# Kernel tuning notes

Measured on AMD Instinct MI355X. Metric: run time of the kernel, lower is better.

## Reference

```python
import jax, jax.numpy as jnp
import numpy as np

NL, D, NH, HD, MLP, L = 4, 1280, 16, 80, 5120, 2048
SEG = 512  # patches per packed image


def setup_inputs() -> dict:
    key = jax.random.key(0)
    ks = jax.random.split(key, 16)
    s = 0.02
    # per-segment RoPE frequency table: positions restart at each image boundary
    inv_freq = 1.0 / (10000.0 ** (jnp.arange(0, HD, 2, dtype=jnp.float32) / HD))  # (HD/2,)
    pos = (jnp.arange(L) % SEG).astype(jnp.float32)
    rotary_pos_emb = pos[:, None] * inv_freq[None, :]  # (L, HD/2)
    return {
        "x": jax.random.normal(ks[0], (L, D), jnp.float32),
        "rotary_pos_emb": rotary_pos_emb,
        "cu_seqlens": jnp.array([0, 512, 1024, 1536, 2048], jnp.int32),
        "ln1_g": 1.0 + s * jax.random.normal(ks[1], (NL, D), jnp.float32),
        "ln1_b": s * jax.random.normal(ks[2], (NL, D), jnp.float32),
        "ln2_g": 1.0 + s * jax.random.normal(ks[3], (NL, D), jnp.float32),
        "ln2_b": s * jax.random.normal(ks[4], (NL, D), jnp.float32),
        "qkv_w": s * jax.random.normal(ks[5], (NL, 3 * D, D), jnp.float32),
        "qkv_b": s * jax.random.normal(ks[6], (NL, 3 * D), jnp.float32),
        "proj_w": s * jax.random.normal(ks[7], (NL, D, D), jnp.float32),
        "proj_b": s * jax.random.normal(ks[8], (NL, D), jnp.float32),
        "mlp_w1": s * jax.random.normal(ks[9], (NL, MLP, D), jnp.float32),
        "mlp_b1": s * jax.random.normal(ks[10], (NL, MLP), jnp.float32),
        "mlp_w2": s * jax.random.normal(ks[11], (NL, D, MLP), jnp.float32),
        "mlp_b2": s * jax.random.normal(ks[12], (NL, D), jnp.float32),
    }


def _ln(x, g, b):
    m = jnp.mean(x, axis=-1, keepdims=True)
    v = jnp.mean((x - m) ** 2, axis=-1, keepdims=True)
    return (x - m) * jax.lax.rsqrt(v + 1e-6) * g + b


def _rope(t, cos, sin):
    # t: (L, H, HD); cos/sin: (L, 1, HD)
    half = t.shape[-1] // 2
    rot = jnp.concatenate([-t[..., half:], t[..., :half]], axis=-1)
    return t * cos + rot * sin


def reference(x, rotary_pos_emb, cu_seqlens, ln1_g, ln1_b, ln2_g, ln2_b,
              qkv_w, qkv_b, proj_w, proj_b, mlp_w1, mlp_b1, mlp_w2, mlp_b2):
    Lx = x.shape[0]
    cos = jnp.cos(rotary_pos_emb)
    sin = jnp.sin(rotary_pos_emb)
    cos = jnp.concatenate([cos, cos], axis=-1)[:, None, :]  # (L,1,HD)
    sin = jnp.concatenate([sin, sin], axis=-1)[:, None, :]
    # block-diagonal attention mask from cu_seqlens via segment ids
    seg = jnp.searchsorted(cu_seqlens, jnp.arange(Lx), side="right")  # (L,)
    mask = seg[:, None] == seg[None, :]  # (L,L) bool
    neg = jnp.finfo(jnp.float32).min
    scale = 1.0 / np.sqrt(HD)
    for l in range(qkv_w.shape[0]):
        h = _ln(x, ln1_g[l], ln1_b[l])
        qkv = (h @ qkv_w[l].T + qkv_b[l]).reshape(Lx, 3, NH, HD)
        q, k, v = qkv[:, 0], qkv[:, 1], qkv[:, 2]  # (L,H,HD) each
        q = _rope(q, cos, sin)
        k = _rope(k, cos, sin)
        scores = jnp.einsum("lhd,mhd->hlm", q, k) * scale  # (H,L,L)
        scores = jnp.where(mask[None], scores, neg)
        w = jax.nn.softmax(scores.astype(jnp.float32), axis=-1).astype(x.dtype)
        att = jnp.einsum("hlm,mhd->lhd", w, v).reshape(Lx, NH * HD)
        x = x + att @ proj_w[l].T + proj_b[l]
        h = _ln(x, ln2_g[l], ln2_b[l])
        x = x + jax.nn.gelu(h @ mlp_w1[l].T + mlp_b1[l], approximate=True) @ mlp_w2[l].T + mlp_b2[l]
    return x
```

## Files before the change

### kernel.cpp

```cpp
#include <hip/hip_runtime.h>
#include <cstdint>
#include <cstddef>

typedef unsigned short u16;
typedef __bf16 bf16_t;
typedef bf16_t bf16x8 __attribute__((ext_vector_type(8)));
typedef float f32x4 __attribute__((ext_vector_type(4)));

#define NLAY 4
#define DMODEL 1280
#define NHEAD 16
#define HDIM 80
#define HDP 96
#define MLPD 5120
#define LTOK 2048
#define SEGLEN 512

__device__ __forceinline__ u16 f2bf(float f) {
  union { float f; unsigned u; } x; x.f = f;
  unsigned r = x.u + 0x7fffu + ((x.u >> 16) & 1u);
  return (u16)(r >> 16);
}
__device__ __forceinline__ float bf2f(u16 s) {
  union { unsigned u; float f; } x; x.u = ((unsigned)s) << 16;
  return x.f;
}

#define GLOAD_LDS16(gsrc, ldst) \
  __builtin_amdgcn_global_load_lds((const __attribute__((address_space(1))) void*)(gsrc), \
                                   (__attribute__((address_space(3))) void*)(ldst), 16, 0, 0)

__device__ __forceinline__ void barrier_mem() {
  asm volatile("s_barrier" ::: "memory");
}

#define C0 (3 * DMODEL * DMODEL / 4)
#define C1 (C0 + DMODEL * DMODEL / 4)
#define C2 (C1 + MLPD * DMODEL / 4)
#define C3 (C2 + DMODEL * MLPD / 4)
__global__ __launch_bounds__(256) void cvt4(const float* __restrict__ s_q,
                                            const float* __restrict__ s_p,
                                            const float* __restrict__ s_1,
                                            const float* __restrict__ s_2,
                                            u16* __restrict__ o_q, u16* __restrict__ o_p,
                                            u16* __restrict__ o_1, u16* __restrict__ o_2) {
  int i = blockIdx.x * 256 + threadIdx.x;
  const float* src; u16* dst; int off;
  if (i < C0)      { src = s_q; dst = o_q; off = i; }
  else if (i < C1) { src = s_p; dst = o_p; off = i - C0; }
  else if (i < C2) { src = s_1; dst = o_1; off = i - C1; }
  else if (i < C3) { src = s_2; dst = o_2; off = i - C2; }
  else return;
  const float4 v = reinterpret_cast<const float4*>(src)[off];
  union { u16 s[4]; uint2 u; } o;
  o.s[0] = f2bf(v.x); o.s[1] = f2bf(v.y); o.s[2] = f2bf(v.z); o.s[3] = f2bf(v.w);
  reinterpret_cast<uint2*>(dst)[off] = o.u;
}

__global__ __launch_bounds__(256) void ln_bf16(const float* __restrict__ x,
                                               const float* __restrict__ g,
                                               const float* __restrict__ b,
                                               u16* __restrict__ out) {
  int row = blockIdx.x;
  int t = threadIdx.x;
  const float* xr = x + (size_t)row * DMODEL;
  float v[5]; float s = 0.f, s2 = 0.f;
#pragma unroll
  for (int i = 0; i < 5; i++) { v[i] = xr[t + i * 256]; s += v[i]; s2 += v[i] * v[i]; }
#pragma unroll
  for (int off = 32; off; off >>= 1) { s += __shfl_down(s, off); s2 += __shfl_down(s2, off); }
  __shared__ float ps[4], ps2[4];
  int w = t >> 6;
  if ((t & 63) == 0) { ps[w] = s; ps2[w] = s2; }
  __syncthreads();
  s = ps[0] + ps[1] + ps[2] + ps[3];
  s2 = ps2[0] + ps2[1] + ps2[2] + ps2[3];
  float mean = s * (1.f / DMODEL);
  float var = s2 * (1.f / DMODEL) - mean * mean;
  float inv = rsqrtf(var + 1e-6f);
#pragma unroll
  for (int i = 0; i < 5; i++) {
    int c = t + i * 256;
    out[(size_t)row * DMODEL + c] = f2bf((v[i] - mean) * inv * g[c] + b[c]);
  }
}

__global__ __launch_bounds__(256) void reduce_ln(const u16* __restrict__ P,
                                                 const float* __restrict__ bias,
                                                 float* __restrict__ x,
                                                 const float* __restrict__ g,
                                                 const float* __restrict__ b,
                                                 u16* __restrict__ out) {
  int row = blockIdx.x;
  int t = threadIdx.x;
  const size_t PS = (size_t)LTOK * DMODEL;
  const size_t base = (size_t)row * DMODEL;
  float v[5]; float s = 0.f, s2 = 0.f;
#pragma unroll
  for (int i = 0; i < 5; i++) {
    int c = t + i * 256;
    float val = x[base + c] + bias[c];
#pragma unroll
    for (int z = 0; z < 4; z++) val += bf2f(P[z * PS + base + c]);
    x[base + c] = val;
    v[i] = val; s += val; s2 += val * val;
  }
#pragma unroll
  for (int off = 32; off; off >>= 1) { s += __shfl_down(s, off); s2 += __shfl_down(s2, off); }
  __shared__ float ps[4], ps2[4];
  int w = t >> 6;
  if ((t & 63) == 0) { ps[w] = s; ps2[w] = s2; }
  __syncthreads();
  s = ps[0] + ps[1] + ps[2] + ps[3];
  s2 = ps2[0] + ps2[1] + ps2[2] + ps2[3];
  float mean = s * (1.f / DMODEL);
  float var = s2 * (1.f / DMODEL) - mean * mean;
  float inv = rsqrtf(var + 1e-6f);
#pragma unroll
  for (int i = 0; i < 5; i++) {
    int c = t + i * 256;
    out[base + c] = f2bf((v[i] - mean) * inv * g[c] + b[c]);
  }
}

template <int EPI>
__global__ __launch_bounds__(512, 4) void gemmhp(const u16* __restrict__ A,
                                                 const u16* __restrict__ B,
                                                 const float* __restrict__ bias,
                                                 u16* __restrict__ Cb,
                                                 int M, int N, int K) {
  __shared__ u16 As[3][128 * 32];
  __shared__ u16 Bs[3][256 * 32];

  int gN = gridDim.x, gM = gridDim.y;
  int flat = blockIdx.x + gN * blockIdx.y;
  int nwg = gN * gM;
  int qc = nwg >> 3, rc = nwg & 7;
  int xcd = flat & 7, pos = flat >> 3;
  int start = (xcd < rc) ? xcd * (qc + 1) : rc * (qc + 1) + (xcd - rc) * qc;
  int swz = start + pos;
  int m0 = (swz % gM) * 128;
  int n0 = (swz / gM) * 256;

  int t = threadIdx.x, lane = t & 63, w = t >> 6;
  int wm = w >> 2, wn = w & 3;
  int r = lane & 15, kq = lane >> 4;
  f32x4 acc[4][4] = {};

  auto stageA = [&](int buf, int k0) {
    int row = t >> 2, s = t & 3;
    int ss = s ^ ((row >> 1) & 3);
    GLOAD_LDS16(A + (size_t)(m0 + row) * K + k0 + ss * 8, &As[buf][t * 8]);
  };
  auto stageB = [&](int buf, int k0) {
#pragma unroll
    for (int i = 0; i < 2; i++) {
      int chunk = i * 512 + t;
      int row = chunk >> 2, s = chunk & 3;
      int ss = s ^ ((row >> 1) & 3);
      GLOAD_LDS16(B + (size_t)(n0 + row) * K + k0 + ss * 8, &Bs[buf][chunk * 8]);
    }
  };

  int NT = K >> 5;
  stageA(0, 0); stageB(0, 0);
  stageA(1, 32); stageB(1, 32);

  int bt = 0;
  for (int kt = 0; kt < NT; kt++) {
    if (kt == NT - 1) asm volatile("s_waitcnt vmcnt(0)" ::: "memory");
    else              asm volatile("s_waitcnt vmcnt(3)" ::: "memory");
    barrier_mem();
    const u16* as = As[bt];
    const u16* bs = Bs[bt];
    int b2 = bt + 2; if (b2 >= 3) b2 -= 3;
    bool st = (kt + 2) < NT;
    int k2 = (kt + 2) << 5;

    bf16x8 af[4], bfv[4];
#pragma unroll
    for (int i = 0; i < 4; i++) {
      int row = wm * 64 + i * 16 + r;
      int ss = kq ^ ((row >> 1) & 3);
      af[i] = *(const bf16x8*)&as[row * 32 + ss * 8];
    }
#pragma unroll
    for (int j = 0; j < 4; j++) {
      int row = wn * 64 + j * 16 + r;
      int ss = kq ^ ((row >> 1) & 3);
      bfv[j] = *(const bf16x8*)&bs[row * 32 + ss * 8];
    }
    if (st) { stageA(b2, k2); stageB(b2, k2); }
    __builtin_amdgcn_s_setprio(1);
#pragma unroll
    for (int i = 0; i < 4; i++)
#pragma unroll
      for (int j = 0; j < 4; j++)
        acc[i][j] = __builtin_amdgcn_mfma_f32_16x16x32_bf16(af[i], bfv[j], acc[i][j], 0, 0, 0);
    __builtin_amdgcn_s_setprio(0);

    bt++; if (bt == 3) bt = 0;
  }

#pragma unroll
  for (int i = 0; i < 4; i++) {
#pragma unroll
    for (int j = 0; j < 4; j++) {
      int col = n0 + wn * 64 + j * 16 + r;
      float bv = bias[col];
#pragma unroll
      for (int reg = 0; reg < 4; reg++) {
        int rowg = m0 + wm * 64 + i * 16 + kq * 4 + reg;
        float val = acc[i][j][reg] + bv;
        if (EPI == 2) {
          float z2 = -1.5957691216057308f * fmaf(0.044715f * val, val * val, val);
          float gg = val / (1.f + __expf(z2));
          Cb[(size_t)rowg * N + col] = f2bf(gg);
        } else {
          Cb[(size_t)rowg * N + col] = f2bf(val);
        }
      }
    }
  }
}

__global__ __launch_bounds__(256, 3) void gemmskb(const u16* __restrict__ A,
                                                  const u16* __restrict__ B,
                                                  u16* __restrict__ P,
                                                  int M, int N, int K, int KC) {
  __shared__ u16 As[3][128 * 32];
  __shared__ u16 Bs[3][128 * 32];

  int gN = gridDim.x, gM = gridDim.y;
  int flat = blockIdx.x + gN * blockIdx.y;
  int nwg = gN * gM;
  int qc = nwg >> 3, rc = nwg & 7;
  int xcd = flat & 7, pos = flat >> 3;
  int start = (xcd < rc) ? xcd * (qc + 1) : rc * (qc + 1) + (xcd - rc) * qc;
  int swz = start + pos;
  int n0 = (swz % gN) * 128;
  int m0 = (swz / gN) * 128;
  int kbase = blockIdx.z * KC;
  u16* Pz = P + (size_t)blockIdx.z * M * N;

  int t = threadIdx.x, lane = t & 63, w = t >> 6;
  int wm = w >> 1, wn = w & 1;
  int r = lane & 15, kq = lane >> 4;
  f32x4 acc[4][4] = {};

  auto stage = [&](int buf, int k0) {
#pragma unroll
    for (int i = 0; i < 2; i++) {
      int chunk = i * 256 + t;
      int row = chunk >> 2, s = chunk & 3;
      int ss = s ^ ((row >> 1) & 3);
      GLOAD_LDS16(A + (size_t)(m0 + row) * K + k0 + ss * 8, &As[buf][chunk * 8]);
    }
#pragma unroll
    for (int i = 0; i < 2; i++) {
      int chunk = i * 256 + t;
      int row = chunk >> 2, s = chunk & 3;
      int ss = s ^ ((row >> 1) & 3);
      GLOAD_LDS16(B + (size_t)(n0 + row) * K + k0 + ss * 8, &Bs[buf][chunk * 8]);
    }
  };

  int NT = KC >> 5;
  stage(0, kbase);
  stage(1, kbase + 32);

  int bt = 0;
  for (int kt = 0; kt < NT; kt++) {
    if (kt == NT - 1) asm volatile("s_waitcnt vmcnt(0)" ::: "memory");
    else              asm volatile("s_waitcnt vmcnt(4)" ::: "memory");
    barrier_mem();
    const u16* as = As[bt];
    const u16* bs = Bs[bt];
    int b2 = bt + 2; if (b2 >= 3) b2 -= 3;
    bool st = (kt + 2) < NT;
    int k2 = kbase + ((kt + 2) << 5);

    bf16x8 af[4], bfv[4];
#pragma unroll
    for (int i = 0; i < 4; i++) {
      int row = wm * 64 + i * 16 + r;
      int ss = kq ^ ((row >> 1) & 3);
      af[i] = *(const bf16x8*)&as[row * 32 + ss * 8];
    }
#pragma unroll
    for (int j = 0; j < 4; j++) {
      int row = wn * 64 + j * 16 + r;
      int ss = kq ^ ((row >> 1) & 3);
      bfv[j] = *(const bf16x8*)&bs[row * 32 + ss * 8];
    }
    if (st) stage(b2, k2);
    __builtin_amdgcn_s_setprio(1);
#pragma unroll
    for (int i = 0; i < 4; i++)
#pragma unroll
      for (int j = 0; j < 4; j++)
        acc[i][j] = __builtin_amdgcn_mfma_f32_16x16x32_bf16(af[i], bfv[j], acc[i][j], 0, 0, 0);
    __builtin_amdgcn_s_setprio(0);

    bt++; if (bt == 3) bt = 0;
  }

#pragma unroll
  for (int i = 0; i < 4; i++) {
#pragma unroll
    for (int j = 0; j < 4; j++) {
      int col = n0 + wn * 64 + j * 16 + r;
#pragma unroll
      for (int reg = 0; reg < 4; reg++) {
        int rowg = m0 + wm * 64 + i * 16 + kq * 4 + reg;
        Pz[(size_t)rowg * N + col] = f2bf(acc[i][j][reg]);
      }
    }
  }
}

#define N8TOT (LTOK * DMODEL / 8)
__global__ __launch_bounds__(256) void reduce4b(const u16* __restrict__ P,
                                                const float* __restrict__ bias,
                                                float4* __restrict__ x) {
  int i = blockIdx.x * 256 + threadIdx.x;
  if (i >= N8TOT) return;
  const size_t PS = (size_t)LTOK * DMODEL;
  float s[8] = {};
#pragma unroll
  for (int z = 0; z < 4; z++) {
    uint4 pv = *reinterpret_cast<const uint4*>(P + z * PS + (size_t)i * 8);
    const u16* ps = (const u16*)&pv;
#pragma unroll
    for (int e = 0; e < 8; e++) s[e] += bf2f(ps[e]);
  }
  int cb = (i % (DMODEL / 8)) * 8;
  float4 b0 = *reinterpret_cast<const float4*>(bias + cb);
  float4 b1 = *reinterpret_cast<const float4*>(bias + cb + 4);
  float4 xv0 = x[i * 2], xv1 = x[i * 2 + 1];
  xv0.x += s[0] + b0.x; xv0.y += s[1] + b0.y;
  xv0.z += s[2] + b0.z; xv0.w += s[3] + b0.w;
  xv1.x += s[4] + b1.x; xv1.y += s[5] + b1.y;
  xv1.z += s[6] + b1.z; xv1.w += s[7] + b1.w;
  x[i * 2] = xv0; x[i * 2 + 1] = xv1;
}

__global__ __launch_bounds__(256) void rope_pack(const u16* __restrict__ qkv,
                                                 const float* __restrict__ rpe,
                                                 u16* __restrict__ qp,
                                                 u16* __restrict__ kp) {
  int l = blockIdx.x;
  int t = threadIdx.x;
  __shared__ float cs[40], sn[40];
  if (t < 40) {
    float a = rpe[l * 40 + t];
    cs[t] = cosf(a);
    sn[t] = sinf(a);
  }
  __syncthreads();
  const u16* row = qkv + (size_t)l * (3 * DMODEL);
  const float scale = 0.11180339887498949f;
#pragma unroll
  for (int i = 0; i < 5; i++) {
    int e = t + i * 256;
    int h = e / HDIM, d = e - h * HDIM;
    int dm = (d < 40) ? d : d - 40;
    float c = cs[dm], s = sn[dm];
    float qv = bf2f(row[h * HDIM + d]);
    float qr = (d < 40) ? -bf2f(row[h * HDIM + d + 40]) : bf2f(row[h * HDIM + d - 40]);
    qp[((size_t)h * LTOK + l) * HDP + d] = f2bf((qv * c + qr * s) * scale);
    float kv = bf2f(row[DMODEL + h * HDIM + d]);
    float kr = (d < 40) ? -bf2f(row[DMODEL + h * HDIM + d + 40]) : bf2f(row[DMODEL + h * HDIM + d - 40]);
    kp[((size_t)h * LTOK + l) * HDP + d] = f2bf(kv * c + kr * s);
  }
  {
    int h = t >> 4, p = t & 15;
    qp[((size_t)h * LTOK + l) * HDP + HDIM + p] = 0;
    kp[((size_t)h * LTOK + l) * HDP + HDIM + p] = 0;
  }
}

__global__ __launch_bounds__(256) void vtrans(const u16* __restrict__ qkv,
                                              u16* __restrict__ vt) {
  int blk = blockIdx.x;
  int h = blk >> 5, lt = blk & 31;
  int t = threadIdx.x;
  __shared__ u16 ld[64][81];
#pragma unroll
  for (int i = 0; i < 20; i++) {
    int idx = t + i * 256;
    int ll = idx / HDIM, d = idx - ll * HDIM;
    ld[ll][d] = qkv[(size_t)(lt * 64 + ll) * (3 * DMODEL) + 2 * DMODEL + h * HDIM + d];
  }
  __syncthreads();
#pragma unroll
  for (int i = 0; i < 20; i++) {
    int idx = t + i * 256;
    int d = idx >> 6, ll = idx & 63;
    vt[((size_t)h * HDIM + d) * LTOK + lt * 64 + ll] = ld[ll][d];
  }
}

__global__ __launch_bounds__(256) void attn(const u16* __restrict__ qp,
                                            const u16* __restrict__ kp,
                                            const u16* __restrict__ vt,
                                            u16* __restrict__ out) {
  int bid = blockIdx.x;
  int h = bid >> 5;
  int seg = (bid >> 3) & 3;
  int qt = bid & 7;
  int t = threadIdx.x, w = t >> 6, lane = t & 63;
  int r = lane & 15, kq = lane >> 4;
  __shared__ u16 P[4][16][512];
  int seg0 = seg * SEGLEN;
  int q0 = seg0 + qt * 64 + w * 16;

  bf16x8 qf[3];
  const u16* qrow = qp + ((size_t)h * LTOK + q0 + r) * HDP;
#pragma unroll
  for (int kk = 0; kk < 3; kk++) qf[kk] = *(const bf16x8*)(qrow + kk * 32 + kq * 8);

  f32x4 sc[32];
#pragma unroll
  for (int j = 0; j < 32; j++) {
    f32x4 a = {0.f, 0.f, 0.f, 0.f};
    const u16* krow = kp + ((size_t)h * LTOK + seg0 + j * 16 + r) * HDP;
#pragma unroll
    for (int kk = 0; kk < 3; kk++) {
      bf16x8 bfr = *(const bf16x8*)(krow + kk * 32 + kq * 8);
      a = __builtin_amdgcn_mfma_f32_16x16x32_bf16(qf[kk], bfr, a, 0, 0, 0);
    }
    sc[j] = a;
  }

#pragma unroll
  for (int rr = 0; rr < 4; rr++) {
    float m = -1e30f;
#pragma unroll
    for (int j = 0; j < 32; j++) m = fmaxf(m, sc[j][rr]);
#pragma unroll
    for (int off = 1; off < 16; off <<= 1) m = fmaxf(m, __shfl_xor(m, off));
    float s = 0.f;
#pragma unroll
    for (int j = 0; j < 32; j++) { float e = __expf(sc[j][rr] - m); sc[j][rr] = e; s += e; }
#pragma unroll
    for (int off = 1; off < 16; off <<= 1) s += __shfl_xor(s, off);
    float inv = 1.f / s;
#pragma unroll
    for (int j = 0; j < 32; j++)
      P[w][kq * 4 + rr][j * 16 + r] = f2bf(sc[j][rr] * inv);
  }
  __syncthreads();

  f32x4 oc[5] = {};
#pragma unroll
  for (int tt = 0; tt < 16; tt++) {
    bf16x8 a = *(const bf16x8*)&P[w][r][tt * 32 + kq * 8];
#pragma unroll
    for (int n = 0; n < 5; n++) {
      const u16* vrow = vt + ((size_t)h * HDIM + n * 16 + r) * LTOK + seg0 + tt * 32 + kq * 8;
      bf16x8 bfr = *(const bf16x8*)vrow;
      oc[n] = __builtin_amdgcn_mfma_f32_16x16x32_bf16(a, bfr, oc[n], 0, 0, 0);
    }
  }
#pragma unroll
  for (int n = 0; n < 5; n++)
#pragma unroll
    for (int reg = 0; reg < 4; reg++) {
      int l = q0 + kq * 4 + reg;
      out[(size_t)l * DMODEL + h * HDIM + n * 16 + r] = f2bf(oc[n][reg]);
    }
}

extern "C" void kernel_launch(void* const* d_in, const int* in_sizes, int n_in,
                              void* d_out, int out_size, void* d_ws, size_t ws_size,
                              hipStream_t stream) {
  (void)in_sizes; (void)n_in; (void)out_size; (void)ws_size;
  const float* x_in   = (const float*)d_in[0];
  const float* rpe    = (const float*)d_in[1];
  const float* ln1_g  = (const float*)d_in[3];
  const float* ln1_b  = (const float*)d_in[4];
  const float* ln2_g  = (const float*)d_in[5];
  const float* ln2_b  = (const float*)d_in[6];
  const float* qkv_w  = (const float*)d_in[7];
  const float* qkv_b  = (const float*)d_in[8];
  const float* proj_w = (const float*)d_in[9];
  const float* proj_b = (const float*)d_in[10];
  const float* mlp_w1 = (const float*)d_in[11];
  const float* mlp_b1 = (const float*)d_in[12];
  const float* mlp_w2 = (const float*)d_in[13];
  const float* mlp_b2 = (const float*)d_in[14];
  float* x = (float*)d_out;

  char* ws = (char*)d_ws;
  size_t off = 0;
  auto alloc = [&](size_t bytes) -> char* {
    char* p = ws + off;
    off = (off + bytes + 255) & ~(size_t)255;
    return p;
  };
  u16* wq  = (u16*)alloc((size_t)3 * DMODEL * DMODEL * 2);
  u16* wp  = (u16*)alloc((size_t)DMODEL * DMODEL * 2);
  u16* w1  = (u16*)alloc((size_t)MLPD * DMODEL * 2);
  u16* w2  = (u16*)alloc((size_t)DMODEL * MLPD * 2);
  u16* hb  = (u16*)alloc((size_t)LTOK * DMODEL * 2);
  u16* qkvb = (u16*)alloc((size_t)LTOK * 3 * DMODEL * 2);
  u16* qp  = (u16*)alloc((size_t)NHEAD * LTOK * HDP * 2);
  u16* kp  = (u16*)alloc((size_t)NHEAD * LTOK * HDP * 2);
  u16* vt  = (u16*)alloc((size_t)NHEAD * HDIM * LTOK * 2);
  u16* att = (u16*)alloc((size_t)LTOK * DMODEL * 2);
  u16* ge  = (u16*)alloc((size_t)LTOK * MLPD * 2);
  u16* pk_proj = ge;
  u16* pk_mlp2 = hb;

  hipMemcpyAsync(x, x_in, (size_t)LTOK * DMODEL * sizeof(float),
                 hipMemcpyDeviceToDevice, stream);

  for (int l = 0; l < NLAY; l++) {
    cvt4<<<(C3 + 255) / 256, 256, 0, stream>>>(
        qkv_w + (size_t)l * 3 * DMODEL * DMODEL, proj_w + (size_t)l * DMODEL * DMODEL,
        mlp_w1 + (size_t)l * MLPD * DMODEL, mlp_w2 + (size_t)l * DMODEL * MLPD,
        wq, wp, w1, w2);

    if (l == 0)
      ln_bf16<<<LTOK, 256, 0, stream>>>(x, ln1_g, ln1_b, hb);
    gemmhp<3><<<dim3(15, 16), 512, 0, stream>>>(
        hb, wq, qkv_b + (size_t)l * 3 * DMODEL, qkvb, LTOK, 3 * DMODEL, DMODEL);
    rope_pack<<<LTOK, 256, 0, stream>>>(qkvb, rpe, qp, kp);
    vtrans<<<NHEAD * 32, 256, 0, stream>>>(qkvb, vt);
    attn<<<NHEAD * 4 * 8, 256, 0, stream>>>(qp, kp, vt, att);
    gemmskb<<<dim3(10, 16, 4), 256, 0, stream>>>(
        att, wp, pk_proj, LTOK, DMODEL, DMODEL, DMODEL / 4);
    reduce_ln<<<LTOK, 256, 0, stream>>>(
        pk_proj, proj_b + (size_t)l * DMODEL, x,
        ln2_g + (size_t)l * DMODEL, ln2_b + (size_t)l * DMODEL, hb);
    gemmhp<2><<<dim3(20, 16), 512, 0, stream>>>(
        hb, w1, mlp_b1 + (size_t)l * MLPD, ge, LTOK, MLPD, DMODEL);
    gemmskb<<<dim3(10, 16, 4), 256, 0, stream>>>(
        ge, w2, pk_mlp2, LTOK, DMODEL, MLPD, MLPD / 4);
    if (l < NLAY - 1)
      reduce_ln<<<LTOK, 256, 0, stream>>>(
          pk_mlp2, mlp_b2 + (size_t)l * DMODEL, x,
          ln1_g + (size_t)(l + 1) * DMODEL, ln1_b + (size_t)(l + 1) * DMODEL, hb);
    else
      reduce4b<<<(N8TOT + 255) / 256, 256, 0, stream>>>(
          pk_mlp2, mlp_b2 + (size_t)l * DMODEL, (float4*)x);
  }
}
```

Measured before the change: 878.1 us.

## Add 128x128 MLP-up GEMM, grouped tile swizzle, fuse RoPE with V transpose

Three changes. The QKV GEMM now remaps workgroup tiles into 4x3 groups for better L2 reuse. The MLP-up GEMM moves to a new 128x128-tile, 256-thread kernel with 4x4 grouped tile ordering, giving more workgroups (640 vs 320) on the device. The RoPE packing and V transpose kernels are merged into one kernel over (head, 64-token tile), which saves a launch and lets each block compute cos/sin for its own token tile. The trade-offs are that cos/sin are now recomputed once per head, and the smaller GEMM tiles give less operand reuse per workgroup.

```diff
diff --git a/kernel.cpp b/kernel.cpp
--- a/kernel.cpp
+++ b/kernel.cpp
@@ -139,8 +139,12 @@
   int xcd = flat & 7, pos = flat >> 3;
   int start = (xcd < rc) ? xcd * (qc + 1) : rc * (qc + 1) + (xcd - rc) * qc;
   int swz = start + pos;
-  int m0 = (swz % gM) * 128;
-  int n0 = (swz / gM) * 256;
+  int inn = swz % 12, blk = swz / 12;
+  int mi = inn & 3, ni = inn >> 2;
+  int bM = gM >> 2;
+  int bmi = blk % bM, bni = blk / bM;
+  int m0 = (bmi * 4 + mi) * 128;
+  int n0 = (bni * 3 + ni) * 256;
 
   int t = threadIdx.x, lane = t & 63, w = t >> 6;
   int wm = w >> 2, wn = w & 3;
@@ -224,6 +228,113 @@
   }
 }
 
+template <int EPI>
+__global__ __launch_bounds__(256, 3) void gemmdk(const u16* __restrict__ A,
+                                                 const u16* __restrict__ B,
+                                                 const float* __restrict__ bias,
+                                                 u16* __restrict__ Cb,
+                                                 int M, int N, int K) {
+  __shared__ u16 As[3][128 * 32];
+  __shared__ u16 Bs[3][128 * 32];
+
+  int gN = gridDim.x, gM = gridDim.y;
+  int flat = blockIdx.x + gN * blockIdx.y;
+  int nwg = gN * gM;
+  int qc = nwg >> 3, rc = nwg & 7;
+  int xcd = flat & 7, pos = flat >> 3;
+  int start = (xcd < rc) ? xcd * (qc + 1) : rc * (qc + 1) + (xcd - rc) * qc;
+  int swz = start + pos;
+  int inn = swz & 15, blk = swz >> 4;
+  int mi = inn & 3, ni = inn >> 2;
+  int bM = gM >> 2;
+  int bmi = blk % bM, bni = blk / bM;
+  int m0 = (bmi * 4 + mi) * 128;
+  int n0 = (bni * 4 + ni) * 128;
+
+  int t = threadIdx.x, lane = t & 63, w = t >> 6;
+  int wm = w >> 1, wn = w & 1;
+  int r = lane & 15, kq = lane >> 4;
+  f32x4 acc[4][4] = {};
+
+  auto stage = [&](int buf, int k0) {
+#pragma unroll
+    for (int i = 0; i < 2; i++) {
+      int chunk = i * 256 + t;
+      int row = chunk >> 2, s = chunk & 3;
+      int ss = s ^ ((row >> 1) & 3);
+      GLOAD_LDS16(A + (size_t)(m0 + row) * K + k0 + ss * 8, &As[buf][chunk * 8]);
+    }
+#pragma unroll
+    for (int i = 0; i < 2; i++) {
+      int chunk = i * 256 + t;
+      int row = chunk >> 2, s = chunk & 3;
+      int ss = s ^ ((row >> 1) & 3);
+      GLOAD_LDS16(B + (size_t)(n0 + row) * K + k0 + ss * 8, &Bs[buf][chunk * 8]);
+    }
+  };
+
+  int NT = K >> 5;
+  stage(0, 0);
+  stage(1, 32);
+
+  int bt = 0;
+  for (int kt = 0; kt < NT; kt++) {
+    if (kt == NT - 1) asm volatile("s_waitcnt vmcnt(0)" ::: "memory");
+    else              asm volatile("s_waitcnt vmcnt(4)" ::: "memory");
+    barrier_mem();
+    const u16* as = As[bt];
+    const u16* bs = Bs[bt];
+    int b2 = bt + 2; if (b2 >= 3) b2 -= 3;
+    bool st = (kt + 2) < NT;
+    int k2 = (kt + 2) << 5;
+
+    bf16x8 af[4], bfv[4];
+#pragma unroll
+    for (int i = 0; i < 4; i++) {
+      int row = wm * 64 + i * 16 + r;
+      int ss = kq ^ ((row >> 1) & 3);
+      af[i] = *(const bf16x8*)&as[row * 32 + ss * 8];
+    }
+#pragma unroll
+    for (int j = 0; j < 4; j++) {
+      int row = wn * 64 + j * 16 + r;
+      int ss = kq ^ ((row >> 1) & 3);
+      bfv[j] = *(const bf16x8*)&bs[row * 32 + ss * 8];
+    }
+    if (st) stage(b2, k2);
+    __builtin_amdgcn_s_setprio(1);
+#pragma unroll
+    for (int i = 0; i < 4; i++)
+#pragma unroll
+      for (int j = 0; j < 4; j++)
+        acc[i][j] = __builtin_amdgcn_mfma_f32_16x16x32_bf16(af[i], bfv[j], acc[i][j], 0, 0, 0);
+    __builtin_amdgcn_s_setprio(0);
+
+    bt++; if (bt == 3) bt = 0;
+  }
+
+#pragma unroll
+  for (int i = 0; i < 4; i++) {
+#pragma unroll
+    for (int j = 0; j < 4; j++) {
+      int col = n0 + wn * 64 + j * 16 + r;
+      float bv = bias[col];
+#pragma unroll
+      for (int reg = 0; reg < 4; reg++) {
+        int rowg = m0 + wm * 64 + i * 16 + kq * 4 + reg;
+        float val = acc[i][j][reg] + bv;
+        if (EPI == 2) {
+          float z2 = -1.5957691216057308f * fmaf(0.044715f * val, val * val, val);
+          float gg = val / (1.f + __expf(z2));
+          Cb[(size_t)rowg * N + col] = f2bf(gg);
+        } else {
+          Cb[(size_t)rowg * N + col] = f2bf(val);
+        }
+      }
+    }
+  }
+}
+
 __global__ __launch_bounds__(256, 3) void gemmskb(const u16* __restrict__ A,
                                                   const u16* __restrict__ B,
                                                   u16* __restrict__ P,
@@ -345,59 +456,64 @@
   x[i * 2] = xv0; x[i * 2 + 1] = xv1;
 }
 
-__global__ __launch_bounds__(256) void rope_pack(const u16* __restrict__ qkv,
-                                                 const float* __restrict__ rpe,
-                                                 u16* __restrict__ qp,
-                                                 u16* __restrict__ kp) {
-  int l = blockIdx.x;
+__global__ __launch_bounds__(256) void rope_vt(const u16* __restrict__ qkv,
+                                               const float* __restrict__ rpe,
+                                               u16* __restrict__ qp,
+                                               u16* __restrict__ kp,
+                                               u16* __restrict__ vt) {
+  int h = blockIdx.x >> 5;
+  int lt = blockIdx.x & 31;
   int t = threadIdx.x;
-  __shared__ float cs[40], sn[40];
-  if (t < 40) {
-    float a = rpe[l * 40 + t];
-    cs[t] = cosf(a);
-    sn[t] = sinf(a);
+  __shared__ float cs[64][40], sn[64][40];
+  __shared__ u16 vld[64][81];
+  const float scale = 0.11180339887498949f;
+
+#pragma unroll
+  for (int e = 0; e < 10; e++) {
+    int idx = t + e * 256;
+    int ll = idx / 40, dm = idx - ll * 40;
+    float a = rpe[(size_t)(lt * 64 + ll) * 40 + dm];
+    cs[ll][dm] = cosf(a);
+    sn[ll][dm] = sinf(a);
   }
   __syncthreads();
-  const u16* row = qkv + (size_t)l * (3 * DMODEL);
-  const float scale = 0.11180339887498949f;
-#pragma unroll
-  for (int i = 0; i < 5; i++) {
-    int e = t + i * 256;
-    int h = e / HDIM, d = e - h * HDIM;
+
+#pragma unroll
+  for (int e = 0; e < 40; e++) {
+    int idx = t + e * 256;
+    int ll = idx / 160, rem = idx - ll * 160;
+    int which = rem / 80, d = rem - which * 80;
     int dm = (d < 40) ? d : d - 40;
-    float c = cs[dm], s = sn[dm];
-    float qv = bf2f(row[h * HDIM + d]);
-    float qr = (d < 40) ? -bf2f(row[h * HDIM + d + 40]) : bf2f(row[h * HDIM + d - 40]);
-    qp[((size_t)h * LTOK + l) * HDP + d] = f2bf((qv * c + qr * s) * scale);
-    float kv = bf2f(row[DMODEL + h * HDIM + d]);
-    float kr = (d < 40) ? -bf2f(row[DMODEL + h * HDIM + d + 40]) : bf2f(row[DMODEL + h * HDIM + d - 40]);
-    kp[((size_t)h * LTOK + l) * HDP + d] = f2bf(kv * c + kr * s);
-  }
-  {
-    int h = t >> 4, p = t & 15;
-    qp[((size_t)h * LTOK + l) * HDP + HDIM + p] = 0;
-    kp[((size_t)h * LTOK + l) * HDP + HDIM + p] = 0;
-  }
-}
-
-__global__ __launch_bounds__(256) void vtrans(const u16* __restrict__ qkv,
-                                              u16* __restrict__ vt) {
-  int blk = blockIdx.x;
-  int h = blk >> 5, lt = blk & 31;
-  int t = threadIdx.x;
-  __shared__ u16 ld[64][81];
-#pragma unroll
-  for (int i = 0; i < 20; i++) {
-    int idx = t + i * 256;
-    int ll = idx / HDIM, d = idx - ll * HDIM;
-    ld[ll][d] = qkv[(size_t)(lt * 64 + ll) * (3 * DMODEL) + 2 * DMODEL + h * HDIM + d];
+    float c = cs[ll][dm], s = sn[ll][dm];
+    const u16* row = qkv + (size_t)(lt * 64 + ll) * (3 * DMODEL) + which * DMODEL + h * HDIM;
+    float v0 = bf2f(row[d]);
+    float vr = (d < 40) ? -bf2f(row[d + 40]) : bf2f(row[d - 40]);
+    float o = v0 * c + vr * s;
+    if (which == 0) o *= scale;
+    u16* dst = which ? kp : qp;
+    dst[((size_t)h * LTOK + lt * 64 + ll) * HDP + d] = f2bf(o);
+  }
+#pragma unroll
+  for (int e = 0; e < 8; e++) {
+    int idx = t + e * 256;
+    int ll = idx >> 5, rem = idx & 31;
+    int which = rem >> 4, p = rem & 15;
+    u16* dst = which ? kp : qp;
+    dst[((size_t)h * LTOK + lt * 64 + ll) * HDP + HDIM + p] = 0;
+  }
+
+#pragma unroll
+  for (int e = 0; e < 20; e++) {
+    int idx = t + e * 256;
+    int ll = idx / 80, d = idx - ll * 80;
+    vld[ll][d] = qkv[(size_t)(lt * 64 + ll) * (3 * DMODEL) + 2 * DMODEL + h * HDIM + d];
   }
   __syncthreads();
 #pragma unroll
-  for (int i = 0; i < 20; i++) {
-    int idx = t + i * 256;
+  for (int e = 0; e < 20; e++) {
+    int idx = t + e * 256;
     int d = idx >> 6, ll = idx & 63;
-    vt[((size_t)h * HDIM + d) * LTOK + lt * 64 + ll] = ld[ll][d];
+    vt[((size_t)h * HDIM + d) * LTOK + lt * 64 + ll] = vld[ll][d];
   }
 }
 
@@ -526,15 +642,14 @@
       ln_bf16<<<LTOK, 256, 0, stream>>>(x, ln1_g, ln1_b, hb);
     gemmhp<3><<<dim3(15, 16), 512, 0, stream>>>(
         hb, wq, qkv_b + (size_t)l * 3 * DMODEL, qkvb, LTOK, 3 * DMODEL, DMODEL);
-    rope_pack<<<LTOK, 256, 0, stream>>>(qkvb, rpe, qp, kp);
-    vtrans<<<NHEAD * 32, 256, 0, stream>>>(qkvb, vt);
+    rope_vt<<<NHEAD * 32, 256, 0, stream>>>(qkvb, rpe, qp, kp, vt);
     attn<<<NHEAD * 4 * 8, 256, 0, stream>>>(qp, kp, vt, att);
     gemmskb<<<dim3(10, 16, 4), 256, 0, stream>>>(
         att, wp, pk_proj, LTOK, DMODEL, DMODEL, DMODEL / 4);
     reduce_ln<<<LTOK, 256, 0, stream>>>(
         pk_proj, proj_b + (size_t)l * DMODEL, x,
         ln2_g + (size_t)l * DMODEL, ln2_b + (size_t)l * DMODEL, hb);
-    gemmhp<2><<<dim3(20, 16), 512, 0, stream>>>(
+    gemmdk<2><<<dim3(40, 16), 256, 0, stream>>>(
         hb, w1, mlp_b1 + (size_t)l * MLPD, ge, LTOK, MLPD, DMODEL);
     gemmskb<<<dim3(10, 16, 4), 256, 0, stream>>>(
         ge, w2, pk_mlp2, LTOK, DMODEL, MLPD, MLPD / 4);
```

New measurement: 945.2 us. 1.08x slower.
